# Kernel optimization log

Measured on AMD Instinct MI355X. Metric: run time of the kernel, lower is better.

## Reference

```python
import jax, jax.numpy as jnp
import numpy as np

P = 16        # patch size
B = 32        # batch
HW = 224      # image height/width
EMB = 768     # embedding dim
CN = (512, 2048, 8192)  # cluster counts
D = 3 * P * P  # patch feature dim = 768


def setup_inputs() -> dict:
    key = jax.random.key(0)
    ks = jax.random.split(key, 7)
    return {
        "data": jax.random.normal(ks[0], (B, 3, HW, HW), jnp.float32),
        "c0": jax.random.normal(ks[1], (CN[0], D), jnp.float32),
        "c1": jax.random.normal(ks[2], (CN[1], D), jnp.float32),
        "c2": jax.random.normal(ks[3], (CN[2], D), jnp.float32),
        "e0": jax.random.normal(ks[4], (CN[0], EMB), jnp.float32),
        "e1": jax.random.normal(ks[5], (CN[1], EMB), jnp.float32),
        "e2": jax.random.normal(ks[6], (CN[2], EMB), jnp.float32),
    }


def _classify(x, center):
    scores = -2.0 * (x @ center.T) + jnp.sum(center * center, axis=-1)  # [b, n, K]
    cls = jnp.argmin(scores, axis=-1)                                   # [b, n]
    img = center[cls]                                                   # nearest-center gather
    return cls, x - img, img


def reference(data, c0, c1, c2, e0, e1, e2):
    b, c, h, w = data.shape
    hp = h // P
    wp = w // P
    # b c (h hp) (w wp) -> b (h w) (c hp wp)
    x = data.reshape(b, c, hp, P, wp, P).transpose(0, 2, 4, 1, 3, 5).reshape(b, hp * wp, c * P * P)

    cls0, diff, img0 = _classify(x, c0)
    cls1, diff, img1 = _classify(diff, c1)
    cls2, diff, img2 = _classify(diff, c2)

    # reconstruct image from summed center patches: b (h w) (c hp wp) -> b c (h hp) (w wp)
    img_sum = (img0 + img1 + img2).reshape(b, hp, wp, c, P, P).transpose(0, 3, 1, 4, 2, 5).reshape(b, c, h, w)
    # residual: b (h w) c -> b c h w
    diff_out = diff.reshape(b, hp, wp, -1).transpose(0, 3, 1, 2)

    # embedding lookups (the only grad-carrying path in the torch module)
    embed = e0[cls0] + e1[cls1] + e2[cls2]          # [b, hp*wp, EMB]
    embed = embed.reshape(b, hp, wp, -1).transpose(0, 3, 1, 2)  # [b, EMB, hp, wp]

    # quantization branch is under torch.no_grad()
    return (embed, jax.lax.stop_gradient(img_sum), jax.lax.stop_gradient(diff_out))
```

## Files before the change

### kernel.cpp

```cpp
#include <hip/hip_runtime.h>
#include <stdint.h>

#define BATCH 32
#define HWD 224
#define HP 14
#define NP (BATCH * HP * HP)
#define DIM 768
#define K0 512
#define K1 2048
#define K2 8192

typedef unsigned long long ull;
typedef unsigned int uint;
typedef __attribute__((ext_vector_type(8))) short bf16x8;
typedef __attribute__((ext_vector_type(4))) float f32x4;

__device__ __forceinline__ uint fkey(float f) {
    uint u = __float_as_uint(f);
    return (u & 0x80000000u) ? ~u : (u | 0x80000000u);
}
__device__ __forceinline__ short f2bf(float f) {
    uint u = __float_as_uint(f);
    uint r = (u + 0x7fffu + ((u >> 16) & 1u)) >> 16;
    return (short)r;
}
__device__ __forceinline__ float bf2f(short h) {
    return __uint_as_float(((uint)(unsigned short)h) << 16);
}
__device__ __forceinline__ ull umin64(ull a, ull b) { return a < b ? a : b; }
__device__ __forceinline__ ull umax64(ull a, ull b) { return a > b ? a : b; }

__global__ void patchify_split_kernel(const float* __restrict__ data,
                                      short* __restrict__ xh, short* __restrict__ xl) {
    int gid = blockIdx.x * 256 + threadIdx.x;
    int d = gid % DIM;
    int p = gid / DIM;
    int b = p / 196; int t = p % 196; int i = t / 14, j = t % 14;
    int ch = d >> 8; int r = d & 255; int py = r >> 4; int px = r & 15;
    float v = data[((b * 3 + ch) * HWD + i * 16 + py) * HWD + j * 16 + px];
    short h = f2bf(v);
    xh[gid] = h;
    xl[gid] = f2bf(v - bf2f(h));
}

__global__ void cprep_kernel(const float* __restrict__ c, short* __restrict__ ch,
                             float* __restrict__ nrm) {
    int lane = threadIdx.x & 63;
    int row = blockIdx.x * 4 + (threadIdx.x >> 6);
    const float* src = c + (size_t)row * DIM;
    float s = 0.f;
    #pragma unroll
    for (int i = 0; i < 12; ++i) {
        int d = lane + i * 64;
        float v = src[d];
        ch[(size_t)row * DIM + d] = f2bf(v);
        s += v * v;
    }
    #pragma unroll
    for (int off = 32; off; off >>= 1) s += __shfl_xor(s, off, 64);
    if (lane == 0) nrm[row] = s;
}

__global__ __launch_bounds__(256, 3) void classify16(
    const short* __restrict__ xh,
    const short* __restrict__ chv,
    const float* __restrict__ nrm,
    ull* __restrict__ partB, ull* __restrict__ partS2)
{
    constexpr int NHT = 4;
    constexpr int NB = 128;
    constexpr int CH0 = 512;
    constexpr int SLOTS = 1024;
    constexpr int NJ = 4;
    constexpr int GX = NP / 128;
    __shared__ __align__(16) short lds[3 * SLOTS * 8];

    int bx = blockIdx.x, by = blockIdx.y;
    if ((gridDim.y & 7) == 0) {
        int P = blockIdx.x + GX * blockIdx.y;
        int xcd = P & 7;
        int wofs = P >> 3;
        int ypx = gridDim.y >> 3;
        by = xcd * ypx + (wofs % ypx);
        bx = wofs / ypx;
    }

    const int tid = threadIdx.x;
    const int lane = tid & 63;
    const int w = tid >> 6;
    const int wm = w & 1, wn = w >> 1;
    const int pbase = bx * 128;
    const int n0 = by * NB;

    const short* gp[NJ];
    int ls[NJ];
    #pragma unroll
    for (int j = 0; j < NJ; ++j) {
        int g = j * 4 + w;
        const short* base; int rb, sb, t;
        if (g < 8) { base = xh;  rb = pbase; sb = 0;    t = g; }
        else       { base = chv; rb = n0;    sb = CH0;  t = g - 8; }
        gp[j] = base + (size_t)(rb + t * 16 + (lane & 15)) * DIM + ((lane >> 4) * 8);
        ls[j] = sb + t * 64;
    }

    f32x4 acc[4][NHT];
    #pragma unroll
    for (int i = 0; i < 4; ++i)
        #pragma unroll
        for (int u = 0; u < NHT; ++u) acc[i][u] = (f32x4){0.f, 0.f, 0.f, 0.f};

    auto stage = [&](int buf, int kt) {
        const int off = buf * SLOTS;
        #pragma unroll
        for (int j = 0; j < NJ; ++j) {
            __builtin_amdgcn_global_load_lds(
                (const __attribute__((address_space(1))) void*)(gp[j] + kt * 32),
                (__attribute__((address_space(3))) void*)(lds + (size_t)(off + ls[j]) * 8),
                16, 0, 0);
        }
    };
    auto compute = [&](int buf) {
        const bf16x8* Lc = (const bf16x8*)lds + buf * SLOTS;
        bf16x8 fxh[4];
        #pragma unroll
        for (int i = 0; i < 4; ++i)
            fxh[i] = Lc[(wm * 4 + i) * 64 + lane];
        #pragma unroll
        for (int u = 0; u < NHT; ++u) {
            bf16x8 fch = Lc[CH0 + (wn * NHT + u) * 64 + lane];
            #pragma unroll
            for (int i = 0; i < 4; ++i)
                acc[i][u] = __builtin_amdgcn_mfma_f32_16x16x32_bf16(fxh[i], fch, acc[i][u], 0, 0, 0);
        }
    };

    stage(0, 0);
    stage(1, 1);
    asm volatile("s_waitcnt vmcnt(4)" ::: "memory");
    __builtin_amdgcn_s_barrier();
    __builtin_amdgcn_sched_barrier(0);

    #pragma unroll 3
    for (int t = 0; t < 24; ++t) {
        if (t + 2 < 24) stage((t + 2) % 3, t + 2);
        compute(t % 3);
        if (t < 23) {
            if (t + 2 < 24) asm volatile("s_waitcnt vmcnt(4)" ::: "memory");
            else            asm volatile("s_waitcnt vmcnt(0)" ::: "memory");
            __builtin_amdgcn_s_barrier();
            __builtin_amdgcn_sched_barrier(0);
        }
    }

    float nor[NHT]; uint ncol[NHT];
    #pragma unroll
    for (int u = 0; u < NHT; ++u) {
        ncol[u] = (uint)(n0 + (wn * NHT + u) * 16 + (lane & 15));
        nor[u] = nrm[ncol[u]];
    }
    const int pw = 2 * gridDim.y;
    #pragma unroll
    for (int i = 0; i < 4; ++i) {
        #pragma unroll
        for (int reg = 0; reg < 4; ++reg) {
            ull b = ~0ull, s2 = ~0ull;
            #pragma unroll
            for (int u = 0; u < NHT; ++u) {
                float s = fmaf(-2.f, acc[i][u][reg], nor[u]);
                ull pk = ((ull)fkey(s) << 32) | ncol[u];
                ull nb = umin64(b, pk);
                s2 = umin64(s2, umax64(b, pk));
                b = nb;
            }
            #pragma unroll
            for (int off = 1; off <= 8; off <<= 1) {
                ull ob = __shfl_xor(b, off, 64);
                ull os2 = __shfl_xor(s2, off, 64);
                ull nb = umin64(b, ob);
                s2 = umin64(umin64(s2, os2), umax64(b, ob));
                b = nb;
            }
            if ((lane & 15) == 0) {
                int row = pbase + (wm * 4 + i) * 16 + (lane >> 4) * 4 + reg;
                size_t o = (size_t)row * pw + (size_t)by * 2 + wn;
                partB[o] = b;
                partS2[o] = s2;
            }
        }
    }
}

__global__ void merge_rescue_update(
    short* __restrict__ xh, short* __restrict__ xl,
    const float* __restrict__ cent, const float* __restrict__ nrm,
    const ull* __restrict__ partB, const ull* __restrict__ partS2,
    int nsplit, int* __restrict__ cls)
{
    int lane = threadIdx.x & 63;
    int p = blockIdx.x * 4 + (threadIdx.x >> 6);
    ull a = ~0ull, c = ~0ull;
    for (int j = lane; j < nsplit; j += 64) {
        ull b2 = partB[(size_t)p * nsplit + j];
        ull s2b = partS2[(size_t)p * nsplit + j];
        ull na = umin64(a, b2);
        c = umin64(umin64(c, s2b), umax64(a, b2));
        a = na;
    }
    int idx[4];
    #pragma unroll
    for (int r = 0; r < 4; ++r) {
        ull m = a;
        #pragma unroll
        for (int off = 32; off; off >>= 1) m = umin64(m, __shfl_xor(m, off, 64));
        idx[r] = (int)(m & 0xFFFFFFFFull);
        if (a == m) { a = c; c = ~0ull; }
    }
    float xv[12];
    #pragma unroll
    for (int i = 0; i < 12; ++i) {
        int d = lane + i * 64;
        xv[i] = bf2f(xh[(size_t)p * DIM + d]) + bf2f(xl[(size_t)p * DIM + d]);
    }
    float dot[4] = {0.f, 0.f, 0.f, 0.f};
    #pragma unroll
    for (int r = 0; r < 4; ++r) {
        const float* cr = cent + (size_t)idx[r] * DIM;
        #pragma unroll
        for (int i = 0; i < 12; ++i) dot[r] = fmaf(xv[i], cr[lane + i * 64], dot[r]);
    }
    #pragma unroll
    for (int r = 0; r < 4; ++r)
        #pragma unroll
        for (int off = 32; off; off >>= 1) dot[r] += __shfl_xor(dot[r], off, 64);
    ull best = ~0ull;
    #pragma unroll
    for (int r = 0; r < 4; ++r) {
        float sc = fmaf(-2.f, dot[r], nrm[idx[r]]);
        best = umin64(best, ((ull)fkey(sc) << 32) | (uint)idx[r]);
    }
    int cw = (int)(best & 0xFFFFFFFFull);
    if (lane == 0) cls[p] = cw;
    const float* cwr = cent + (size_t)cw * DIM;
    #pragma unroll
    for (int i = 0; i < 12; ++i) {
        int d = lane + i * 64;
        float nx = xv[i] - cwr[d];
        short h = f2bf(nx);
        xh[(size_t)p * DIM + d] = h;
        xl[(size_t)p * DIM + d] = f2bf(nx - bf2f(h));
    }
}

__global__ void embdiff_kernel(const short* __restrict__ xh, const short* __restrict__ xl,
    const int* __restrict__ cls0, const int* __restrict__ cls1, const int* __restrict__ cls2,
    const float* __restrict__ e0, const float* __restrict__ e1, const float* __restrict__ e2,
    float* __restrict__ out)
{
    __shared__ float s[196][65];
    int b = blockIdx.x / 12;
    int dc = (blockIdx.x % 12) * 64;
    int tid = threadIdx.x;
    int dl = tid & 63;
    for (int it = 0; it < 49; ++it) {
        int pl = it * 4 + (tid >> 6);
        int p = b * 196 + pl;
        int d = dc + dl;
        s[pl][dl] = e0[(size_t)cls0[p] * DIM + d] + e1[(size_t)cls1[p] * DIM + d]
                  + e2[(size_t)cls2[p] * DIM + d];
    }
    __syncthreads();
    if (tid < 196) {
        for (int d = 0; d < 64; ++d)
            out[((size_t)b * DIM + dc + d) * 196 + tid] = s[tid][d];
    }
    __syncthreads();
    for (int it = 0; it < 49; ++it) {
        int pl = it * 4 + (tid >> 6);
        size_t o = (size_t)(b * 196 + pl) * DIM + dc + dl;
        s[pl][dl] = bf2f(xh[o]) + bf2f(xl[o]);
    }
    __syncthreads();
    if (tid < 196) {
        float* od = out + 2 * (size_t)NP * DIM;
        for (int d = 0; d < 64; ++d)
            od[((size_t)b * DIM + dc + d) * 196 + tid] = s[tid][d];
    }
}

__global__ void img_kernel(
    const int* __restrict__ cls0, const int* __restrict__ cls1, const int* __restrict__ cls2,
    const float* __restrict__ c0, const float* __restrict__ c1, const float* __restrict__ c2,
    float* __restrict__ out)
{
    __shared__ float s[14][256];
    int bi = blockIdx.x;
    int b = bi / 42; int rem = bi % 42; int ch = rem / 14; int i = rem % 14;
    int tid = threadIdx.x;
    for (int j = 0; j < 14; ++j) {
        int p = b * 196 + i * 14 + j;
        int d = ch * 256 + tid;
        s[j][tid] = c0[(size_t)cls0[p] * DIM + d] + c1[(size_t)cls1[p] * DIM + d]
                  + c2[(size_t)cls2[p] * DIM + d];
    }
    __syncthreads();
    float* oi = out + (size_t)NP * DIM;
    if (tid < 224) {
        int j = tid >> 4, px = tid & 15;
        for (int py = 0; py < 16; ++py)
            oi[(((size_t)b * 3 + ch) * HWD + i * 16 + py) * HWD + tid] = s[j][py * 16 + px];
    }
}

extern "C" void kernel_launch(void* const* d_in, const int* in_sizes, int n_in,
                              void* d_out, int out_size, void* d_ws, size_t ws_size,
                              hipStream_t stream) {
    const float* data = (const float*)d_in[0];
    const float* c0 = (const float*)d_in[1];
    const float* c1 = (const float*)d_in[2];
    const float* c2 = (const float*)d_in[3];
    const float* e0 = (const float*)d_in[4];
    const float* e1 = (const float*)d_in[5];
    const float* e2 = (const float*)d_in[6];
    float* out = (float*)d_out;

    char* w = (char*)d_ws;
    short* xh = (short*)w;    w += (size_t)NP * DIM * 2;
    short* xl = (short*)w;    w += (size_t)NP * DIM * 2;
    short* chB = (short*)w;   w += (size_t)K2 * DIM * 2;
    float* nrm = (float*)w;   w += (size_t)K2 * 4;
    ull* partB = (ull*)w;     w += (size_t)NP * 128 * 8;
    ull* partS2 = (ull*)w;    w += (size_t)NP * 128 * 8;
    int* cls0 = (int*)w;      w += (size_t)NP * 4;
    int* cls1 = (int*)w;      w += (size_t)NP * 4;
    int* cls2 = (int*)w;      w += (size_t)NP * 4;

    patchify_split_kernel<<<(NP * DIM) / 256, 256, 0, stream>>>(data, xh, xl);

    cprep_kernel<<<K0 / 4, 256, 0, stream>>>(c0, chB, nrm);
    classify16<<<dim3(NP / 128, K0 / 128), 256, 0, stream>>>(xh, chB, nrm, partB, partS2);
    merge_rescue_update<<<NP / 4, 256, 0, stream>>>(xh, xl, c0, nrm, partB, partS2, 8, cls0);

    cprep_kernel<<<K1 / 4, 256, 0, stream>>>(c1, chB, nrm);
    classify16<<<dim3(NP / 128, K1 / 128), 256, 0, stream>>>(xh, chB, nrm, partB, partS2);
    merge_rescue_update<<<NP / 4, 256, 0, stream>>>(xh, xl, c1, nrm, partB, partS2, 32, cls1);

    cprep_kernel<<<K2 / 4, 256, 0, stream>>>(c2, chB, nrm);
    classify16<<<dim3(NP / 128, K2 / 128), 256, 0, stream>>>(xh, chB, nrm, partB, partS2);
    merge_rescue_update<<<NP / 4, 256, 0, stream>>>(xh, xl, c2, nrm, partB, partS2, 128, cls2);

    embdiff_kernel<<<BATCH * 12, 256, 0, stream>>>(xh, xl, cls0, cls1, cls2, e0, e1, e2, out);
    img_kernel<<<BATCH * 3 * 14, 256, 0, stream>>>(cls0, cls1, cls2, c0, c1, c2, out);
}
```

Baseline: 458.7 us.

## Widen classify tile to 256 centers, load X fragments directly into registers

The classify GEMM tile grows from 128x128 to 128x256 (points x centers), each wave now covering 64x128. The X operand is read straight from global memory into register double-buffers rather than staged through LDS, and only the center tile goes through LDS, which moves from triple to double buffering with a K-step of 64. The aim is to raise MFMA work per byte loaded, halve the number of partial argmin results the merge pass must read, and cut LDS traffic. In exchange there are more accumulator registers (occupancy hint lowered from 3 to 2 blocks), half as many blocks in the grid, and direct global loads of X that may expose more latency.

```diff
diff --git a/kernel.cpp b/kernel.cpp
--- a/kernel.cpp
+++ b/kernel.cpp
@@ -61,19 +61,16 @@
     if (lane == 0) nrm[row] = s;
 }
 
-__global__ __launch_bounds__(256, 3) void classify16(
+__global__ __launch_bounds__(256, 2) void classify16(
     const short* __restrict__ xh,
     const short* __restrict__ chv,
     const float* __restrict__ nrm,
     ull* __restrict__ partB, ull* __restrict__ partS2)
 {
-    constexpr int NHT = 4;
-    constexpr int NB = 128;
-    constexpr int CH0 = 512;
-    constexpr int SLOTS = 1024;
-    constexpr int NJ = 4;
+    constexpr int SLOTS = 2048;
+    constexpr int NJ = 8;
     constexpr int GX = NP / 128;
-    __shared__ __align__(16) short lds[3 * SLOTS * 8];
+    __shared__ __align__(16) short lds[2 * SLOTS * 8];
 
     int bx = blockIdx.x, by = blockIdx.y;
     if ((gridDim.y & 7) == 0) {
@@ -90,73 +87,83 @@
     const int w = tid >> 6;
     const int wm = w & 1, wn = w >> 1;
     const int pbase = bx * 128;
-    const int n0 = by * NB;
+    const int n0 = by * 256;
 
     const short* gp[NJ];
     int ls[NJ];
     #pragma unroll
     for (int j = 0; j < NJ; ++j) {
         int g = j * 4 + w;
-        const short* base; int rb, sb, t;
-        if (g < 8) { base = xh;  rb = pbase; sb = 0;    t = g; }
-        else       { base = chv; rb = n0;    sb = CH0;  t = g - 8; }
-        gp[j] = base + (size_t)(rb + t * 16 + (lane & 15)) * DIM + ((lane >> 4) * 8);
-        ls[j] = sb + t * 64;
-    }
-
-    f32x4 acc[4][NHT];
+        gp[j] = chv + (size_t)(n0 + (g & 15) * 16 + (lane & 15)) * DIM
+                    + (g >> 4) * 32 + ((lane >> 4) * 8);
+        ls[j] = g * 64;
+    }
+    const short* gpA[4];
     #pragma unroll
     for (int i = 0; i < 4; ++i)
-        #pragma unroll
-        for (int u = 0; u < NHT; ++u) acc[i][u] = (f32x4){0.f, 0.f, 0.f, 0.f};
+        gpA[i] = xh + (size_t)(pbase + wm * 64 + i * 16 + (lane & 15)) * DIM
+                    + ((lane >> 4) * 8);
+
+    f32x4 acc[4][8];
+    #pragma unroll
+    for (int i = 0; i < 4; ++i)
+        #pragma unroll
+        for (int u = 0; u < 8; ++u) acc[i][u] = (f32x4){0.f, 0.f, 0.f, 0.f};
+
+    bf16x8 pA[2][8];
 
     auto stage = [&](int buf, int kt) {
-        const int off = buf * SLOTS;
         #pragma unroll
         for (int j = 0; j < NJ; ++j) {
             __builtin_amdgcn_global_load_lds(
-                (const __attribute__((address_space(1))) void*)(gp[j] + kt * 32),
-                (__attribute__((address_space(3))) void*)(lds + (size_t)(off + ls[j]) * 8),
+                (const __attribute__((address_space(1))) void*)(gp[j] + kt * 64),
+                (__attribute__((address_space(3))) void*)(lds + (size_t)(buf * SLOTS + ls[j]) * 8),
                 16, 0, 0);
         }
     };
-    auto compute = [&](int buf) {
+    auto loadA = [&](int kt, int s) {
+        #pragma unroll
+        for (int i = 0; i < 4; ++i)
+            #pragma unroll
+            for (int kk = 0; kk < 2; ++kk)
+                pA[s][i * 2 + kk] = *(const bf16x8*)(gpA[i] + kt * 64 + kk * 32);
+    };
+    auto compute = [&](int buf, int s) {
         const bf16x8* Lc = (const bf16x8*)lds + buf * SLOTS;
-        bf16x8 fxh[4];
-        #pragma unroll
-        for (int i = 0; i < 4; ++i)
-            fxh[i] = Lc[(wm * 4 + i) * 64 + lane];
-        #pragma unroll
-        for (int u = 0; u < NHT; ++u) {
-            bf16x8 fch = Lc[CH0 + (wn * NHT + u) * 64 + lane];
+        #pragma unroll
+        for (int kk = 0; kk < 2; ++kk)
             #pragma unroll
-            for (int i = 0; i < 4; ++i)
-                acc[i][u] = __builtin_amdgcn_mfma_f32_16x16x32_bf16(fxh[i], fch, acc[i][u], 0, 0, 0);
+            for (int u = 0; u < 8; ++u) {
+                bf16x8 fch = Lc[(kk * 16 + wn * 8 + u) * 64 + lane];
+                #pragma unroll
+                for (int i = 0; i < 4; ++i)
+                    acc[i][u] = __builtin_amdgcn_mfma_f32_16x16x32_bf16(
+                        pA[s][i * 2 + kk], fch, acc[i][u], 0, 0, 0);
+            }
+    };
+
+    stage(0, 0);
+    loadA(0, 0);
+    asm volatile("s_waitcnt vmcnt(8)" ::: "memory");
+    __builtin_amdgcn_s_barrier();
+
+    #pragma unroll
+    for (int t = 0; t < 12; ++t) {
+        if (t + 1 < 12) {
+            stage((t + 1) & 1, t + 1);
+            loadA(t + 1, (t + 1) & 1);
         }
-    };
-
-    stage(0, 0);
-    stage(1, 1);
-    asm volatile("s_waitcnt vmcnt(4)" ::: "memory");
-    __builtin_amdgcn_s_barrier();
-    __builtin_amdgcn_sched_barrier(0);
-
-    #pragma unroll 3
-    for (int t = 0; t < 24; ++t) {
-        if (t + 2 < 24) stage((t + 2) % 3, t + 2);
-        compute(t % 3);
-        if (t < 23) {
-            if (t + 2 < 24) asm volatile("s_waitcnt vmcnt(4)" ::: "memory");
-            else            asm volatile("s_waitcnt vmcnt(0)" ::: "memory");
+        compute(t & 1, t & 1);
+        if (t < 11) {
+            asm volatile("s_waitcnt vmcnt(8)" ::: "memory");
             __builtin_amdgcn_s_barrier();
-            __builtin_amdgcn_sched_barrier(0);
         }
     }
 
-    float nor[NHT]; uint ncol[NHT];
-    #pragma unroll
-    for (int u = 0; u < NHT; ++u) {
-        ncol[u] = (uint)(n0 + (wn * NHT + u) * 16 + (lane & 15));
+    float nor[8]; uint ncol[8];
+    #pragma unroll
+    for (int u = 0; u < 8; ++u) {
+        ncol[u] = (uint)(n0 + (wn * 8 + u) * 16 + (lane & 15));
         nor[u] = nrm[ncol[u]];
     }
     const int pw = 2 * gridDim.y;
@@ -166,7 +173,7 @@
         for (int reg = 0; reg < 4; ++reg) {
             ull b = ~0ull, s2 = ~0ull;
             #pragma unroll
-            for (int u = 0; u < NHT; ++u) {
+            for (int u = 0; u < 8; ++u) {
                 float s = fmaf(-2.f, acc[i][u][reg], nor[u]);
                 ull pk = ((ull)fkey(s) << 32) | ncol[u];
                 ull nb = umin64(b, pk);
@@ -182,7 +189,7 @@
                 b = nb;
             }
             if ((lane & 15) == 0) {
-                int row = pbase + (wm * 4 + i) * 16 + (lane >> 4) * 4 + reg;
+                int row = pbase + wm * 64 + i * 16 + (lane >> 4) * 4 + reg;
                 size_t o = (size_t)row * pw + (size_t)by * 2 + wn;
                 partB[o] = b;
                 partS2[o] = s2;
@@ -338,16 +345,16 @@
     patchify_split_kernel<<<(NP * DIM) / 256, 256, 0, stream>>>(data, xh, xl);
 
     cprep_kernel<<<K0 / 4, 256, 0, stream>>>(c0, chB, nrm);
-    classify16<<<dim3(NP / 128, K0 / 128), 256, 0, stream>>>(xh, chB, nrm, partB, partS2);
-    merge_rescue_update<<<NP / 4, 256, 0, stream>>>(xh, xl, c0, nrm, partB, partS2, 8, cls0);
+    classify16<<<dim3(NP / 128, K0 / 256), 256, 0, stream>>>(xh, chB, nrm, partB, partS2);
+    merge_rescue_update<<<NP / 4, 256, 0, stream>>>(xh, xl, c0, nrm, partB, partS2, 4, cls0);
 
     cprep_kernel<<<K1 / 4, 256, 0, stream>>>(c1, chB, nrm);
-    classify16<<<dim3(NP / 128, K1 / 128), 256, 0, stream>>>(xh, chB, nrm, partB, partS2);
-    merge_rescue_update<<<NP / 4, 256, 0, stream>>>(xh, xl, c1, nrm, partB, partS2, 32, cls1);
+    classify16<<<dim3(NP / 128, K1 / 256), 256, 0, stream>>>(xh, chB, nrm, partB, partS2);
+    merge_rescue_update<<<NP / 4, 256, 0, stream>>>(xh, xl, c1, nrm, partB, partS2, 16, cls1);
 
     cprep_kernel<<<K2 / 4, 256, 0, stream>>>(c2, chB, nrm);
-    classify16<<<dim3(NP / 128, K2 / 128), 256, 0, stream>>>(xh, chB, nrm, partB, partS2);
-    merge_rescue_update<<<NP / 4, 256, 0, stream>>>(xh, xl, c2, nrm, partB, partS2, 128, cls2);
+    classify16<<<dim3(NP / 128, K2 / 256), 256, 0, stream>>>(xh, chB, nrm, partB, partS2);
+    merge_rescue_update<<<NP / 4, 256, 0, stream>>>(xh, xl, c2, nrm, partB, partS2, 64, cls2);
 
     embdiff_kernel<<<BATCH * 12, 256, 0, stream>>>(xh, xl, cls0, cls1, cls2, e0, e1, e2, out);
     img_kernel<<<BATCH * 3 * 14, 256, 0, stream>>>(cls0, cls1, cls2, c0, c1, c2, out);
```

Result: slower. 520.8 us (+13.5%).

## Template classify kernel on M tile, use double buffering, smaller tiles for small codebooks

Applied to the files above, without the earlier changes.

Makes the classify GEMM kernel a template over the number of 16-row M sub-tiles per warp. The small codebooks (512, 2048) now launch with 64-row patch tiles so the grid has more blocks. The LDS pipeline drops from triple to double buffering with plain __syncthreads, and launch bounds rise to 5 blocks per CU for higher occupancy. The cost is less load/compute overlap per block and more barrier stalls, which may hurt the large 8192 stage.

```diff
diff --git a/kernel.cpp b/kernel.cpp
--- a/kernel.cpp
+++ b/kernel.cpp
@@ -61,19 +61,18 @@
     if (lane == 0) nrm[row] = s;
 }
 
-__global__ __launch_bounds__(256, 3) void classify16(
+template<int MH>
+__global__ __launch_bounds__(256, 5) void classify16(
     const short* __restrict__ xh,
     const short* __restrict__ chv,
     const float* __restrict__ nrm,
     ull* __restrict__ partB, ull* __restrict__ partS2)
 {
-    constexpr int NHT = 4;
-    constexpr int NB = 128;
-    constexpr int CH0 = 512;
-    constexpr int SLOTS = 1024;
-    constexpr int NJ = 4;
-    constexpr int GX = NP / 128;
-    __shared__ __align__(16) short lds[3 * SLOTS * 8];
+    constexpr int CH0 = MH * 128;
+    constexpr int SLOTS = CH0 + 512;
+    constexpr int NJ = (2 * MH + 8) / 4;
+    constexpr int GX = NP / (MH * 32);
+    __shared__ __align__(16) short lds[2 * SLOTS * 8];
 
     int bx = blockIdx.x, by = blockIdx.y;
     if ((gridDim.y & 7) == 0) {
@@ -89,8 +88,8 @@
     const int lane = tid & 63;
     const int w = tid >> 6;
     const int wm = w & 1, wn = w >> 1;
-    const int pbase = bx * 128;
-    const int n0 = by * NB;
+    const int pbase = bx * (MH * 32);
+    const int n0 = by * 128;
 
     const short* gp[NJ];
     int ls[NJ];
@@ -98,17 +97,17 @@
     for (int j = 0; j < NJ; ++j) {
         int g = j * 4 + w;
         const short* base; int rb, sb, t;
-        if (g < 8) { base = xh;  rb = pbase; sb = 0;    t = g; }
-        else       { base = chv; rb = n0;    sb = CH0;  t = g - 8; }
+        if (g < 2 * MH) { base = xh;  rb = pbase; sb = 0;    t = g; }
+        else            { base = chv; rb = n0;    sb = CH0;  t = g - 2 * MH; }
         gp[j] = base + (size_t)(rb + t * 16 + (lane & 15)) * DIM + ((lane >> 4) * 8);
         ls[j] = sb + t * 64;
     }
 
-    f32x4 acc[4][NHT];
-    #pragma unroll
-    for (int i = 0; i < 4; ++i)
-        #pragma unroll
-        for (int u = 0; u < NHT; ++u) acc[i][u] = (f32x4){0.f, 0.f, 0.f, 0.f};
+    f32x4 acc[MH][4];
+    #pragma unroll
+    for (int i = 0; i < MH; ++i)
+        #pragma unroll
+        for (int u = 0; u < 4; ++u) acc[i][u] = (f32x4){0.f, 0.f, 0.f, 0.f};
 
     auto stage = [&](int buf, int kt) {
         const int off = buf * SLOTS;
@@ -122,51 +121,42 @@
     };
     auto compute = [&](int buf) {
         const bf16x8* Lc = (const bf16x8*)lds + buf * SLOTS;
-        bf16x8 fxh[4];
-        #pragma unroll
-        for (int i = 0; i < 4; ++i)
-            fxh[i] = Lc[(wm * 4 + i) * 64 + lane];
-        #pragma unroll
-        for (int u = 0; u < NHT; ++u) {
-            bf16x8 fch = Lc[CH0 + (wn * NHT + u) * 64 + lane];
+        bf16x8 fxh[MH];
+        #pragma unroll
+        for (int i = 0; i < MH; ++i)
+            fxh[i] = Lc[(wm * MH + i) * 64 + lane];
+        #pragma unroll
+        for (int u = 0; u < 4; ++u) {
+            bf16x8 fch = Lc[CH0 + (wn * 4 + u) * 64 + lane];
             #pragma unroll
-            for (int i = 0; i < 4; ++i)
+            for (int i = 0; i < MH; ++i)
                 acc[i][u] = __builtin_amdgcn_mfma_f32_16x16x32_bf16(fxh[i], fch, acc[i][u], 0, 0, 0);
         }
     };
 
     stage(0, 0);
-    stage(1, 1);
-    asm volatile("s_waitcnt vmcnt(4)" ::: "memory");
-    __builtin_amdgcn_s_barrier();
-    __builtin_amdgcn_sched_barrier(0);
-
-    #pragma unroll 3
+    __syncthreads();
+    #pragma unroll 4
     for (int t = 0; t < 24; ++t) {
-        if (t + 2 < 24) stage((t + 2) % 3, t + 2);
-        compute(t % 3);
-        if (t < 23) {
-            if (t + 2 < 24) asm volatile("s_waitcnt vmcnt(4)" ::: "memory");
-            else            asm volatile("s_waitcnt vmcnt(0)" ::: "memory");
-            __builtin_amdgcn_s_barrier();
-            __builtin_amdgcn_sched_barrier(0);
-        }
-    }
-
-    float nor[NHT]; uint ncol[NHT];
-    #pragma unroll
-    for (int u = 0; u < NHT; ++u) {
-        ncol[u] = (uint)(n0 + (wn * NHT + u) * 16 + (lane & 15));
+        if (t + 1 < 24) stage((t + 1) & 1, t + 1);
+        compute(t & 1);
+        if (t < 23) __syncthreads();
+    }
+
+    float nor[4]; uint ncol[4];
+    #pragma unroll
+    for (int u = 0; u < 4; ++u) {
+        ncol[u] = (uint)(n0 + (wn * 4 + u) * 16 + (lane & 15));
         nor[u] = nrm[ncol[u]];
     }
     const int pw = 2 * gridDim.y;
     #pragma unroll
-    for (int i = 0; i < 4; ++i) {
+    for (int i = 0; i < MH; ++i) {
         #pragma unroll
         for (int reg = 0; reg < 4; ++reg) {
             ull b = ~0ull, s2 = ~0ull;
             #pragma unroll
-            for (int u = 0; u < NHT; ++u) {
+            for (int u = 0; u < 4; ++u) {
                 float s = fmaf(-2.f, acc[i][u][reg], nor[u]);
                 ull pk = ((ull)fkey(s) << 32) | ncol[u];
                 ull nb = umin64(b, pk);
@@ -182,7 +172,7 @@
                 b = nb;
             }
             if ((lane & 15) == 0) {
-                int row = pbase + (wm * 4 + i) * 16 + (lane >> 4) * 4 + reg;
+                int row = pbase + (wm * MH + i) * 16 + (lane >> 4) * 4 + reg;
                 size_t o = (size_t)row * pw + (size_t)by * 2 + wn;
                 partB[o] = b;
                 partS2[o] = s2;
@@ -338,15 +328,15 @@
     patchify_split_kernel<<<(NP * DIM) / 256, 256, 0, stream>>>(data, xh, xl);
 
     cprep_kernel<<<K0 / 4, 256, 0, stream>>>(c0, chB, nrm);
-    classify16<<<dim3(NP / 128, K0 / 128), 256, 0, stream>>>(xh, chB, nrm, partB, partS2);
+    classify16<2><<<dim3(NP / 64, K0 / 128), 256, 0, stream>>>(xh, chB, nrm, partB, partS2);
     merge_rescue_update<<<NP / 4, 256, 0, stream>>>(xh, xl, c0, nrm, partB, partS2, 8, cls0);
 
     cprep_kernel<<<K1 / 4, 256, 0, stream>>>(c1, chB, nrm);
-    classify16<<<dim3(NP / 128, K1 / 128), 256, 0, stream>>>(xh, chB, nrm, partB, partS2);
+    classify16<2><<<dim3(NP / 64, K1 / 128), 256, 0, stream>>>(xh, chB, nrm, partB, partS2);
     merge_rescue_update<<<NP / 4, 256, 0, stream>>>(xh, xl, c1, nrm, partB, partS2, 32, cls1);
 
     cprep_kernel<<<K2 / 4, 256, 0, stream>>>(c2, chB, nrm);
-    classify16<<<dim3(NP / 128, K2 / 128), 256, 0, stream>>>(xh, chB, nrm, partB, partS2);
+    classify16<4><<<dim3(NP / 128, K2 / 128), 256, 0, stream>>>(xh, chB, nrm, partB, partS2);
     merge_rescue_update<<<NP / 4, 256, 0, stream>>>(xh, xl, c2, nrm, partB, partS2, 128, cls2);
 
     embdiff_kernel<<<BATCH * 12, 256, 0, stream>>>(xh, xl, cls0, cls1, cls2, e0, e1, e2, out);
```

Result: slower. 665.5 us (+45.1%).
